# Performance work log

Hardware: AMD Instinct MI355X
Metric: run time of the kernel (lower is better)

The kernel has to match this reference:

```python
import jax, jax.numpy as jnp
import numpy as np

N, E, K, D = 100000, 3200000, 1024, 11


def setup_inputs() -> dict:
    key = jax.random.key(0)
    ks = jax.random.split(key, 11)
    return {
        "x": jax.random.normal(ks[0], (N, D), jnp.float32),
        "edge_index": jax.random.randint(ks[1], (2, E), 0, N, dtype=jnp.int32),
        "ready_idx": jnp.sort(jax.random.randint(ks[2], (K,), 0, N, dtype=jnp.int32)),
        "W1": jax.random.normal(ks[3], (D, 64), jnp.float32) * 0.2,
        "b1": jax.random.normal(ks[4], (64,), jnp.float32) * 0.02,
        "W2": jax.random.normal(ks[5], (75, 1), jnp.float32) * 0.2,
        "b2": jax.random.normal(ks[6], (1,), jnp.float32) * 0.02,
        "Wd": jax.random.normal(ks[7], (64, 1), jnp.float32) * 0.2,
        "bd": jax.random.normal(ks[8], (1,), jnp.float32) * 0.02,
        "Wv": jax.random.normal(ks[9], (64, 1), jnp.float32) * 0.2,
        "bv": jax.random.normal(ks[10], (1,), jnp.float32) * 0.02,
    }


def gcn_conv(x, W, b, src, dst):
    """PyG GCNConv with flow='target_to_source': gather from dst, aggregate at src.
    Symmetric normalization with self-loops (weight 1)."""
    n = x.shape[0]
    h = x @ W  # [N, F_out]
    loop = jnp.arange(n, dtype=src.dtype)
    s = jnp.concatenate([src, loop])  # aggregation index (row for target_to_source)
    d = jnp.concatenate([dst, loop])  # gather index
    deg = jax.ops.segment_sum(jnp.ones(s.shape, h.dtype), s, num_segments=n)
    dis = jnp.where(deg > 0, jax.lax.rsqrt(jnp.maximum(deg, 1e-12)), 0.0)
    norm = dis[s] * dis[d]  # [E+N]
    out = jax.ops.segment_sum(norm[:, None] * h[d], s, num_segments=n)
    return out + b


def reference(x, edge_index, ready_idx, W1, b1, W2, b2, Wd, bd, Wv, bv):
    src, dst = edge_index[0], edge_index[1]
    h = jax.nn.relu(gcn_conv(x, W1, b1, src, dst))           # [N, 64]
    x_input = jnp.concatenate([h, x], axis=1)                # [N, 75]
    probs_n = gcn_conv(x_input, W2, b2, src, dst)            # [N, 1]
    x_mean = jnp.mean(h, axis=0)                             # [64]
    v = x_mean @ Wv + bv                                     # [1]
    prob_nothing = x_mean @ Wd + bd                          # [1]
    logits = jnp.concatenate([probs_n[ready_idx, 0], prob_nothing])  # [K+1]
    probs = jax.nn.softmax(logits)
    return probs, v
```

## Files before the change

### kernel.cpp

```cpp
#include <hip/hip_runtime.h>
#include <hip/hip_fp16.h>
#include <math.h>

#define N_ 100000
#define E_ 3200000
#define K_ 1024
#define D_ 11
#define NBUCK_ 391
#define NPAD_ (NBUCK_ * 256)
#define CAPB_ 16384
#define CAP_ 32
#define CAPW_ 33
#define GB_ 512
#define BT_ 1024
#define CHUNK_ 6256
#define SA_ 4
#define XC_ 32
#define RSEG_ 4096
#define RSTRIDE_ 16

static inline size_t align512(size_t x) { return (x + 511) & ~(size_t)511; }

__device__ inline float2 h2f(unsigned int u) {
    __half2 h = *reinterpret_cast<__half2*>(&u);
    return __half22float2(h);
}

__global__ __launch_bounds__(BT_) void k_bin(const int* __restrict__ src,
                                             const int* __restrict__ dst,
                                             int* __restrict__ bcur,
                                             int* __restrict__ gbuf) {
    __shared__ int sbuf[NBUCK_ * CAPW_];
    __shared__ int scnt[NBUCK_];
    int t = threadIdx.x;
    for (int b = t; b < NBUCK_; b += BT_) scnt[b] = 0;
    __syncthreads();
    long e0 = (long)blockIdx.x * CHUNK_;
    for (int r = 0; r < CHUNK_; r += BT_ * 8) {
        int off = r + t * 8;
        long i0 = e0 + off;
        if (off < CHUNK_ && i0 + 7 < E_) {
            int4 s0 = *(const int4*)(src + i0);
            int4 s1 = *(const int4*)(src + i0 + 4);
            int4 d0 = *(const int4*)(dst + i0);
            int4 d1 = *(const int4*)(dst + i0 + 4);
            int ss[8] = {s0.x, s0.y, s0.z, s0.w, s1.x, s1.y, s1.z, s1.w};
            int dd[8] = {d0.x, d0.y, d0.z, d0.w, d1.x, d1.y, d1.z, d1.w};
#pragma unroll
            for (int q = 0; q < 8; q++) {
                int b = ss[q] >> 8;
                int pack = ((ss[q] & 255) << 17) | dd[q];
                int pos = atomicAdd(&scnt[b], 1);
                if (pos < CAP_) sbuf[b * CAPW_ + pos] = pack;
                else gbuf[b * CAPB_ + atomicAdd(&bcur[b], 1)] = pack;
            }
        }
    }
    __syncthreads();
    for (int b = t; b < NBUCK_; b += BT_) {
        int c = min(scnt[b], CAP_);
        while (c >= 16) {
            int off = atomicAdd(&bcur[b], 16);
            int g = b * CAPB_ + off;
            c -= 16;
            if ((off & 3) == 0) {
                int4* gp = (int4*)(gbuf + g);
#pragma unroll
                for (int q = 0; q < 4; q++)
                    gp[q] = make_int4(sbuf[b*CAPW_ + c + 4*q],
                                      sbuf[b*CAPW_ + c + 4*q + 1],
                                      sbuf[b*CAPW_ + c + 4*q + 2],
                                      sbuf[b*CAPW_ + c + 4*q + 3]);
            } else {
                for (int k = 0; k < 16; k++) gbuf[g + k] = sbuf[b*CAPW_ + c + k];
            }
        }
        if (c > 0) {
            int g = b * CAPB_ + atomicAdd(&bcur[b], c);
            for (int k = 0; k < c; k++) gbuf[g + k] = sbuf[b*CAPW_ + k];
        }
    }
}

__global__ __launch_bounds__(1024) void k_deg(const int* __restrict__ bcur,
                                              const int* __restrict__ gbuf,
                                              const float* __restrict__ x,
                                              const int* __restrict__ ready,
                                              float* __restrict__ dis,
                                              __half* __restrict__ xh,
                                              unsigned char* __restrict__ flag,
                                              float* __restrict__ pr_raw,
                                              float* __restrict__ xpart,
                                              int* __restrict__ rcntp) {
    __shared__ int hist[256];
    int t = threadIdx.x, b = blockIdx.x;
    if (t < 256) hist[t] = 0;
    int gi = b * 1024 + t;
    if (gi < XC_ * 64) xpart[gi] = 0.f;
    if (gi < 32 * RSTRIDE_) rcntp[gi] = 0;
    __syncthreads();
    int base = b * CAPB_;
    int cnt = min(bcur[b], CAPB_);
    int p = t * 4;
    for (; p + 3 < cnt; p += 4096) {
        int4 v = *(const int4*)(gbuf + base + p);
        atomicAdd(&hist[v.x >> 17], 1);
        atomicAdd(&hist[v.y >> 17], 1);
        atomicAdd(&hist[v.z >> 17], 1);
        atomicAdd(&hist[v.w >> 17], 1);
    }
    if (p < cnt) {
        for (int q = p; q < cnt; q++) atomicAdd(&hist[gbuf[base + q] >> 17], 1);
    }
    __syncthreads();
    if (t < 256) {
        int node = (b << 8) + t;
        if (node < N_) {
            float dv = rsqrtf((float)(hist[t] + 1));
            dis[node] = dv;
            pr_raw[node] = 0.f;
            __half hh[16];
#pragma unroll
            for (int j = 0; j < D_; j++)
                hh[j] = __float2half_rn(x[(size_t)node * D_ + j]);
            hh[11] = __float2half_rn(dv);
#pragma unroll
            for (int j = 12; j < 16; j++) hh[j] = __float2half_rn(0.f);
            uint4* dst = (uint4*)(xh + (size_t)node * 16);
            dst[0] = *(uint4*)(hh);
            dst[1] = *(uint4*)(hh + 8);
            int lo = 0, hi = K_ - 1, f = 0;
            while (lo <= hi) {
                int mid = (lo + hi) >> 1;
                int v = ready[mid];
                if (v == node) { f = 1; break; }
                if (v < node) lo = mid + 1; else hi = mid - 1;
            }
            flag[node] = (unsigned char)f;
        }
    }
}

__global__ __launch_bounds__(256) void k_agg(const int* __restrict__ bcur,
                                             const int* __restrict__ gbuf,
                                             const __half* __restrict__ xh,
                                             const unsigned char* __restrict__ flag,
                                             float* __restrict__ upart,
                                             int* __restrict__ rcntp,
                                             int2* __restrict__ redge) {
    __shared__ int sorted[4096];
    __shared__ int hist[256];
    __shared__ int incl[256];
    __shared__ int offa[256];
    int t = threadIdx.x, b = blockIdx.x, s = blockIdx.y;
    hist[t] = 0;
    __syncthreads();
    int base = b * CAPB_;
    int cnt = min(bcur[b], CAPB_);
    int seg = (cnt + SA_ - 1) / SA_;
    int lo = s * seg, hi = min(lo + seg, cnt);
    int segn = hi - lo;
    int kmax = (segn + 255) >> 8;
    int pk[16], rk[16];
    for (int k = 0; k < kmax; k++) {
        int idx = lo + (k << 8) + t;
        if (idx < hi) {
            pk[k] = gbuf[base + idx];
            rk[k] = atomicAdd(&hist[pk[k] >> 17], 1);
        } else pk[k] = -1;
    }
    __syncthreads();
    incl[t] = hist[t];
    __syncthreads();
    for (int off = 1; off < 256; off <<= 1) {
        int v = (t >= off) ? incl[t - off] : 0;
        __syncthreads();
        incl[t] += v;
        __syncthreads();
    }
    offa[t] = incl[t] - hist[t];
    __syncthreads();
    for (int k = 0; k < kmax; k++) {
        if (pk[k] >= 0) sorted[offa[pk[k] >> 17] + rk[k]] = pk[k];
    }
    __syncthreads();
    int my_start = offa[t], my_cnt = hist[t];
    int node = (b << 8) + t;
    const uint4* xr = (const uint4*)xh;
    float acc[D_];
#pragma unroll
    for (int j = 0; j < D_; j++) acc[j] = 0.f;
    int i = 0;
    for (; i + 3 < my_cnt; i += 4) {
        int pp[4];
#pragma unroll
        for (int q = 0; q < 4; q++) pp[q] = sorted[my_start + i + q];
        uint4 A[4], B[4];
#pragma unroll
        for (int q = 0; q < 4; q++) {
            size_t r = (size_t)(pp[q] & 131071) * 2;
            A[q] = xr[r]; B[q] = xr[r + 1];
        }
#pragma unroll
        for (int q = 0; q < 4; q++) {
            float2 f0 = h2f(A[q].x), f1 = h2f(A[q].y), f2 = h2f(A[q].z);
            float2 f3 = h2f(A[q].w), f4 = h2f(B[q].x), f5 = h2f(B[q].y);
            float w = f5.y;
            acc[0]  = fmaf(w, f0.x, acc[0]);
            acc[1]  = fmaf(w, f0.y, acc[1]);
            acc[2]  = fmaf(w, f1.x, acc[2]);
            acc[3]  = fmaf(w, f1.y, acc[3]);
            acc[4]  = fmaf(w, f2.x, acc[4]);
            acc[5]  = fmaf(w, f2.y, acc[5]);
            acc[6]  = fmaf(w, f3.x, acc[6]);
            acc[7]  = fmaf(w, f3.y, acc[7]);
            acc[8]  = fmaf(w, f4.x, acc[8]);
            acc[9]  = fmaf(w, f4.y, acc[9]);
            acc[10] = fmaf(w, f5.x, acc[10]);
        }
    }
    for (; i < my_cnt; i++) {
        int pack = sorted[my_start + i];
        size_t r = (size_t)(pack & 131071) * 2;
        uint4 A = xr[r], B = xr[r + 1];
        float2 f0 = h2f(A.x), f1 = h2f(A.y), f2 = h2f(A.z);
        float2 f3 = h2f(A.w), f4 = h2f(B.x), f5 = h2f(B.y);
        float w = f5.y;
        acc[0]  = fmaf(w, f0.x, acc[0]);
        acc[1]  = fmaf(w, f0.y, acc[1]);
        acc[2]  = fmaf(w, f1.x, acc[2]);
        acc[3]  = fmaf(w, f1.y, acc[3]);
        acc[4]  = fmaf(w, f2.x, acc[4]);
        acc[5]  = fmaf(w, f2.y, acc[5]);
        acc[6]  = fmaf(w, f3.x, acc[6]);
        acc[7]  = fmaf(w, f3.y, acc[7]);
        acc[8]  = fmaf(w, f4.x, acc[8]);
        acc[9]  = fmaf(w, f4.y, acc[9]);
        acc[10] = fmaf(w, f5.x, acc[10]);
    }
    float* dst = upart + ((size_t)s * NPAD_ + node) * 12;
    ((float4*)dst)[0] = make_float4(acc[0], acc[1], acc[2],  acc[3]);
    ((float4*)dst)[1] = make_float4(acc[4], acc[5], acc[6],  acc[7]);
    ((float4*)dst)[2] = make_float4(acc[8], acc[9], acc[10], 0.f);

    if (node < N_ && my_cnt > 0 && flag[node]) {
        int r = (b * SA_ + s) & 31;
        int slot = atomicAdd(&rcntp[r * RSTRIDE_], my_cnt);
        int lim = min(my_cnt, max(0, RSEG_ - slot));
        for (int i2 = 0; i2 < lim; i2++)
            redge[(r << 12) + slot + i2] =
                make_int2(node, sorted[my_start + i2] & 131071);
    }
}

__global__ __launch_bounds__(256) void k_node(
    const float* __restrict__ upart, const float* __restrict__ x,
    const float* __restrict__ dis,
    const float* __restrict__ W1, const float* __restrict__ b1,
    const float* __restrict__ W2,
    float* __restrict__ hd, float* __restrict__ xpart) {
    __shared__ float sW1[D_ * 64];
    __shared__ float sb1[64];
    __shared__ float sW2[75];
    __shared__ float smean[64];
    int t = threadIdx.x;
    for (int k = t; k < D_ * 64; k += 256) sW1[k] = W1[k];
    if (t < 64) { sb1[t] = b1[t]; smean[t] = 0.f; }
    if (t < 75) sW2[t] = W2[t];
    __syncthreads();

    int nl = t >> 2, q = t & 3;
    int node = blockIdx.x * 64 + nl;
    bool valid = node < N_;

    float4 mine = make_float4(0.f, 0.f, 0.f, 0.f);
    if (valid && q < 3) {
        const int TOT3 = NPAD_ * 3;
        int slot = node * 3 + q;
        const float4* up = (const float4*)upart;
        float4 a = up[slot];
#pragma unroll
        for (int s = 1; s < SA_; s++) {
            float4 v = up[(size_t)s * TOT3 + slot];
            a.x += v.x; a.y += v.y; a.z += v.z; a.w += v.w;
        }
        mine = a;
    }
    int lb = (t & 63) & ~3;
    float acc[D_];
    acc[0]  = __shfl(mine.x, lb);     acc[1]  = __shfl(mine.y, lb);
    acc[2]  = __shfl(mine.z, lb);     acc[3]  = __shfl(mine.w, lb);
    acc[4]  = __shfl(mine.x, lb + 1); acc[5]  = __shfl(mine.y, lb + 1);
    acc[6]  = __shfl(mine.z, lb + 1); acc[7]  = __shfl(mine.w, lb + 1);
    acc[8]  = __shfl(mine.x, lb + 2); acc[9]  = __shfl(mine.y, lb + 2);
    acc[10] = __shfl(mine.z, lb + 2);

    float hreg[16];
    float h2v = 0.f;
    float di = 0.f;
    if (valid) {
        di = dis[node];
        float xr_[D_], g[D_];
#pragma unroll
        for (int j = 0; j < D_; j++) xr_[j] = x[(size_t)node * D_ + j];
#pragma unroll
        for (int j = 0; j < D_; j++) g[j] = di * (acc[j] + di * xr_[j]);

        int fbase = q << 4;
#pragma unroll
        for (int j = 0; j < 16; j++) {
            int f = fbase + j;
            float a = sb1[f];
#pragma unroll
            for (int jj = 0; jj < D_; jj++) a = fmaf(g[jj], sW1[jj * 64 + f], a);
            float hf = fmaxf(a, 0.f);
            hreg[j] = hf;
            h2v = fmaf(hf, sW2[f], h2v);
        }
        if (q == 0) {
#pragma unroll
            for (int jj = 0; jj < D_; jj++) h2v = fmaf(xr_[jj], sW2[64 + jj], h2v);
        }
    } else {
#pragma unroll
        for (int j = 0; j < 16; j++) hreg[j] = 0.f;
    }
    h2v += __shfl_xor(h2v, 1);
    h2v += __shfl_xor(h2v, 2);
    if (valid && q == 0) hd[node] = di * h2v;

    int lane = t & 63;
#pragma unroll
    for (int j = 0; j < 16; j++) {
        float v = hreg[j];
        v += __shfl_xor(v, 4);
        v += __shfl_xor(v, 8);
        v += __shfl_xor(v, 16);
        v += __shfl_xor(v, 32);
        if (lane < 4) atomicAdd(&smean[(lane << 4) + j], v);
    }
    __syncthreads();
    if (t < 64) atomicAdd(&xpart[((blockIdx.x & (XC_ - 1)) << 6) + t], smean[t]);
}

__global__ void k_pr(const int* __restrict__ rcntp, const int2* __restrict__ redge,
                     const float* __restrict__ hd, float* __restrict__ pr_raw) {
    int idx = blockIdx.x * blockDim.x + threadIdx.x;
    int r = idx >> 12;
    int off = idx & (RSEG_ - 1);
    if (r < 32 && off < min(rcntp[r * RSTRIDE_], RSEG_)) {
        int2 e = redge[(r << 12) + off];
        atomicAdd(&pr_raw[e.x], hd[e.y]);
    }
}

__global__ __launch_bounds__(1024) void k_final(
    const int* __restrict__ ready, const float* __restrict__ dis,
    const float* __restrict__ hd, const float* __restrict__ pr_raw,
    const float* __restrict__ xpart,
    const float* __restrict__ b2,
    const float* __restrict__ Wd, const float* __restrict__ bd,
    const float* __restrict__ Wv, const float* __restrict__ bv,
    float* __restrict__ out) {
    __shared__ float xm[64];
    __shared__ float red[1024];
    __shared__ float s_max, s_sum, s_pn, s_v;
    int t = threadIdx.x;
    if (t < 64) {
        float s = 0.f;
#pragma unroll
        for (int c = 0; c < XC_; c++) s += xpart[(c << 6) + t];
        xm[t] = s * (1.0f / N_);
    }
    __syncthreads();
    if (t == 0) {
        float pn = bd[0], vv = bv[0];
        for (int f = 0; f < 64; f++) { pn += xm[f] * Wd[f]; vv += xm[f] * Wv[f]; }
        s_pn = pn; s_v = vv;
    }
    int r = ready[t];
    float dr = dis[r];
    float l = dr * (pr_raw[r] + hd[r]) + b2[0];
    __syncthreads();
    float pn = s_pn;
    red[t] = (t == 0) ? fmaxf(l, pn) : l;
    __syncthreads();
    for (int sft = 512; sft > 0; sft >>= 1) {
        if (t < sft) red[t] = fmaxf(red[t], red[t + sft]);
        __syncthreads();
    }
    if (t == 0) s_max = red[0];
    __syncthreads();
    float m = s_max;
    float el = expf(l - m);
    red[t] = el + ((t == 0) ? expf(pn - m) : 0.f);
    __syncthreads();
    for (int sft = 512; sft > 0; sft >>= 1) {
        if (t < sft) red[t] += red[t + sft];
        __syncthreads();
    }
    if (t == 0) s_sum = red[0];
    __syncthreads();
    float inv = 1.0f / s_sum;
    out[t] = el * inv;
    if (t == 0) {
        out[K_] = expf(pn - m) * inv;
        out[K_ + 1] = s_v;
    }
}

extern "C" void kernel_launch(void* const* d_in, const int* in_sizes, int n_in,
                              void* d_out, int out_size, void* d_ws, size_t ws_size,
                              hipStream_t stream) {
    const float* x    = (const float*)d_in[0];
    const int*   ei   = (const int*)d_in[1];
    const int*   src  = ei;
    const int*   dst  = ei + E_;
    const int*   ready= (const int*)d_in[2];
    const float* W1   = (const float*)d_in[3];
    const float* b1   = (const float*)d_in[4];
    const float* W2   = (const float*)d_in[5];
    const float* b2   = (const float*)d_in[6];
    const float* Wd   = (const float*)d_in[7];
    const float* bd   = (const float*)d_in[8];
    const float* Wv   = (const float*)d_in[9];
    const float* bv   = (const float*)d_in[10];
    float* out = (float*)d_out;

    char* ws = (char*)d_ws;
    size_t o = 0;
    int*   bcur   = (int*)(ws + o);          o += align512(NBUCK_ * sizeof(int));
    int*   rcntp  = (int*)(ws + o);          o += align512(32 * RSTRIDE_ * sizeof(int));
    int*   gbuf   = (int*)(ws + o);          o += align512((size_t)NBUCK_ * CAPB_ * sizeof(int));
    float* upart  = (float*)(ws + o);        o += align512((size_t)SA_ * NPAD_ * 12 * sizeof(float));
    __half* xh    = (__half*)(ws + o);       o += align512((size_t)N_ * 16 * sizeof(__half));
    int2*  redge  = (int2*)(ws + o);         o += align512((size_t)32 * RSEG_ * sizeof(int2));
    float* dis    = (float*)(ws + o);        o += align512(N_ * sizeof(float));
    float* hd     = (float*)(ws + o);        o += align512(N_ * sizeof(float));
    float* pr_raw = (float*)(ws + o);        o += align512(N_ * sizeof(float));
    unsigned char* flag = (unsigned char*)(ws + o); o += align512(N_);
    float* xpart  = (float*)(ws + o);        o += align512(XC_ * 64 * sizeof(float));

    const int B = 256;
    int g_node4 = (N_ + 63) / 64;
    int g_pr    = (32 * RSEG_) / B;
    dim3 gagg(NBUCK_, SA_);

    hipMemsetAsync(bcur, 0, NBUCK_ * sizeof(int), stream);
    k_bin  <<<GB_, BT_, 0, stream>>>(src, dst, bcur, gbuf);
    k_deg  <<<NBUCK_, 1024, 0, stream>>>(bcur, gbuf, x, ready, dis, xh, flag,
                                         pr_raw, xpart, rcntp);
    k_agg  <<<gagg, B, 0, stream>>>(bcur, gbuf, xh, flag, upart, rcntp, redge);
    k_node <<<g_node4, B, 0, stream>>>(upart, x, dis, W1, b1, W2, hd, xpart);
    k_pr   <<<g_pr, B, 0, stream>>>(rcntp, redge, hd, pr_raw);
    k_final<<<1, 1024, 0, stream>>>(ready, dis, hd, pr_raw, xpart,
                                    b2, Wd, bd, Wv, bv, out);
}
```

Baseline: 189.3 us.

## Fuse aggregation and node MLP into one 1024-thread per-bucket kernel

Merges k_agg and k_node into one kernel, k_agx. Each 1024-thread block handles a whole bucket of 256 nodes, with four threads per node splitting that node's edges and combining their partial sums through shuffles. This removes the upart partial-sum buffer (its write and re-read through global memory) and one kernel launch. It also recomputes the normalization from the shared histogram instead of loading dis. In exchange, the grid is only 391 large blocks that each need 64KB of shared memory for the sort buffer, which may limit occupancy. The sort switches to a two-pass scheme that reads gbuf twice.

```diff
diff --git a/kernel.cpp b/kernel.cpp
--- a/kernel.cpp
+++ b/kernel.cpp
@@ -14,7 +14,6 @@
 #define GB_ 512
 #define BT_ 1024
 #define CHUNK_ 6256
-#define SA_ 4
 #define XC_ 32
 #define RSEG_ 4096
 #define RSTRIDE_ 16
@@ -141,88 +140,62 @@
     }
 }
 
-__global__ __launch_bounds__(256) void k_agg(const int* __restrict__ bcur,
-                                             const int* __restrict__ gbuf,
-                                             const __half* __restrict__ xh,
-                                             const unsigned char* __restrict__ flag,
-                                             float* __restrict__ upart,
-                                             int* __restrict__ rcntp,
-                                             int2* __restrict__ redge) {
-    __shared__ int sorted[4096];
+__global__ __launch_bounds__(1024, 8) void k_agx(
+    const int* __restrict__ bcur, const int* __restrict__ gbuf,
+    const __half* __restrict__ xh, const float* __restrict__ x,
+    const unsigned char* __restrict__ flag,
+    const float* __restrict__ W1, const float* __restrict__ b1,
+    const float* __restrict__ W2,
+    float* __restrict__ hd, float* __restrict__ xpart,
+    int* __restrict__ rcntp, int2* __restrict__ redge) {
+    __shared__ int sorted[CAPB_];
     __shared__ int hist[256];
     __shared__ int incl[256];
     __shared__ int offa[256];
-    int t = threadIdx.x, b = blockIdx.x, s = blockIdx.y;
-    hist[t] = 0;
+    __shared__ int cur[256];
+    __shared__ float sW1[D_ * 64];
+    __shared__ float sb1[64];
+    __shared__ float sW2[75];
+    __shared__ float smean[64];
+    int t = threadIdx.x, b = blockIdx.x;
+    if (t < D_ * 64) sW1[t] = W1[t];
+    if (t >= 768 && t < 832) { sb1[t - 768] = b1[t - 768]; smean[t - 768] = 0.f; }
+    if (t >= 832 && t < 907) sW2[t - 832] = W2[t - 832];
+    if (t < 256) hist[t] = 0;
     __syncthreads();
     int base = b * CAPB_;
     int cnt = min(bcur[b], CAPB_);
-    int seg = (cnt + SA_ - 1) / SA_;
-    int lo = s * seg, hi = min(lo + seg, cnt);
-    int segn = hi - lo;
-    int kmax = (segn + 255) >> 8;
-    int pk[16], rk[16];
-    for (int k = 0; k < kmax; k++) {
-        int idx = lo + (k << 8) + t;
-        if (idx < hi) {
-            pk[k] = gbuf[base + idx];
-            rk[k] = atomicAdd(&hist[pk[k] >> 17], 1);
-        } else pk[k] = -1;
-    }
-    __syncthreads();
-    incl[t] = hist[t];
+    for (int idx = t; idx < cnt; idx += 1024)
+        atomicAdd(&hist[gbuf[base + idx] >> 17], 1);
+    __syncthreads();
+    if (t < 256) incl[t] = hist[t];
     __syncthreads();
     for (int off = 1; off < 256; off <<= 1) {
-        int v = (t >= off) ? incl[t - off] : 0;
+        int v = 0;
+        if (t < 256 && t >= off) v = incl[t - off];
         __syncthreads();
-        incl[t] += v;
+        if (t < 256) incl[t] += v;
         __syncthreads();
     }
-    offa[t] = incl[t] - hist[t];
-    __syncthreads();
-    for (int k = 0; k < kmax; k++) {
-        if (pk[k] >= 0) sorted[offa[pk[k] >> 17] + rk[k]] = pk[k];
-    }
-    __syncthreads();
-    int my_start = offa[t], my_cnt = hist[t];
-    int node = (b << 8) + t;
-    const uint4* xr = (const uint4*)xh;
+    if (t < 256) { int o = incl[t] - hist[t]; offa[t] = o; cur[t] = o; }
+    __syncthreads();
+    for (int idx = t; idx < cnt; idx += 1024) {
+        int pk = gbuf[base + idx];
+        sorted[atomicAdd(&cur[pk >> 17], 1)] = pk;
+    }
+    __syncthreads();
+    int nl = t >> 2, q = t & 3;
+    int node = (b << 8) + nl;
+    bool valid = node < N_;
+    int my_start = offa[nl], my_cnt = hist[nl];
+    const uint4* xr4 = (const uint4*)xh;
     float acc[D_];
 #pragma unroll
     for (int j = 0; j < D_; j++) acc[j] = 0.f;
-    int i = 0;
-    for (; i + 3 < my_cnt; i += 4) {
-        int pp[4];
-#pragma unroll
-        for (int q = 0; q < 4; q++) pp[q] = sorted[my_start + i + q];
-        uint4 A[4], B[4];
-#pragma unroll
-        for (int q = 0; q < 4; q++) {
-            size_t r = (size_t)(pp[q] & 131071) * 2;
-            A[q] = xr[r]; B[q] = xr[r + 1];
-        }
-#pragma unroll
-        for (int q = 0; q < 4; q++) {
-            float2 f0 = h2f(A[q].x), f1 = h2f(A[q].y), f2 = h2f(A[q].z);
-            float2 f3 = h2f(A[q].w), f4 = h2f(B[q].x), f5 = h2f(B[q].y);
-            float w = f5.y;
-            acc[0]  = fmaf(w, f0.x, acc[0]);
-            acc[1]  = fmaf(w, f0.y, acc[1]);
-            acc[2]  = fmaf(w, f1.x, acc[2]);
-            acc[3]  = fmaf(w, f1.y, acc[3]);
-            acc[4]  = fmaf(w, f2.x, acc[4]);
-            acc[5]  = fmaf(w, f2.y, acc[5]);
-            acc[6]  = fmaf(w, f3.x, acc[6]);
-            acc[7]  = fmaf(w, f3.y, acc[7]);
-            acc[8]  = fmaf(w, f4.x, acc[8]);
-            acc[9]  = fmaf(w, f4.y, acc[9]);
-            acc[10] = fmaf(w, f5.x, acc[10]);
-        }
-    }
-    for (; i < my_cnt; i++) {
+    for (int i = q; i < my_cnt; i += 4) {
         int pack = sorted[my_start + i];
         size_t r = (size_t)(pack & 131071) * 2;
-        uint4 A = xr[r], B = xr[r + 1];
+        uint4 A = xr4[r], B = xr4[r + 1];
         float2 f0 = h2f(A.x), f1 = h2f(A.y), f2 = h2f(A.z);
         float2 f3 = h2f(A.w), f4 = h2f(B.x), f5 = h2f(B.y);
         float w = f5.y;
@@ -238,74 +211,25 @@
         acc[9]  = fmaf(w, f4.y, acc[9]);
         acc[10] = fmaf(w, f5.x, acc[10]);
     }
-    float* dst = upart + ((size_t)s * NPAD_ + node) * 12;
-    ((float4*)dst)[0] = make_float4(acc[0], acc[1], acc[2],  acc[3]);
-    ((float4*)dst)[1] = make_float4(acc[4], acc[5], acc[6],  acc[7]);
-    ((float4*)dst)[2] = make_float4(acc[8], acc[9], acc[10], 0.f);
-
-    if (node < N_ && my_cnt > 0 && flag[node]) {
-        int r = (b * SA_ + s) & 31;
-        int slot = atomicAdd(&rcntp[r * RSTRIDE_], my_cnt);
-        int lim = min(my_cnt, max(0, RSEG_ - slot));
-        for (int i2 = 0; i2 < lim; i2++)
-            redge[(r << 12) + slot + i2] =
-                make_int2(node, sorted[my_start + i2] & 131071);
-    }
-}
-
-__global__ __launch_bounds__(256) void k_node(
-    const float* __restrict__ upart, const float* __restrict__ x,
-    const float* __restrict__ dis,
-    const float* __restrict__ W1, const float* __restrict__ b1,
-    const float* __restrict__ W2,
-    float* __restrict__ hd, float* __restrict__ xpart) {
-    __shared__ float sW1[D_ * 64];
-    __shared__ float sb1[64];
-    __shared__ float sW2[75];
-    __shared__ float smean[64];
-    int t = threadIdx.x;
-    for (int k = t; k < D_ * 64; k += 256) sW1[k] = W1[k];
-    if (t < 64) { sb1[t] = b1[t]; smean[t] = 0.f; }
-    if (t < 75) sW2[t] = W2[t];
-    __syncthreads();
-
-    int nl = t >> 2, q = t & 3;
-    int node = blockIdx.x * 64 + nl;
-    bool valid = node < N_;
-
-    float4 mine = make_float4(0.f, 0.f, 0.f, 0.f);
-    if (valid && q < 3) {
-        const int TOT3 = NPAD_ * 3;
-        int slot = node * 3 + q;
-        const float4* up = (const float4*)upart;
-        float4 a = up[slot];
-#pragma unroll
-        for (int s = 1; s < SA_; s++) {
-            float4 v = up[(size_t)s * TOT3 + slot];
-            a.x += v.x; a.y += v.y; a.z += v.z; a.w += v.w;
-        }
-        mine = a;
-    }
-    int lb = (t & 63) & ~3;
-    float acc[D_];
-    acc[0]  = __shfl(mine.x, lb);     acc[1]  = __shfl(mine.y, lb);
-    acc[2]  = __shfl(mine.z, lb);     acc[3]  = __shfl(mine.w, lb);
-    acc[4]  = __shfl(mine.x, lb + 1); acc[5]  = __shfl(mine.y, lb + 1);
-    acc[6]  = __shfl(mine.z, lb + 1); acc[7]  = __shfl(mine.w, lb + 1);
-    acc[8]  = __shfl(mine.x, lb + 2); acc[9]  = __shfl(mine.y, lb + 2);
-    acc[10] = __shfl(mine.z, lb + 2);
-
+#pragma unroll
+    for (int j = 0; j < D_; j++) {
+        acc[j] += __shfl_xor(acc[j], 1);
+        acc[j] += __shfl_xor(acc[j], 2);
+    }
     float hreg[16];
     float h2v = 0.f;
     float di = 0.f;
     if (valid) {
-        di = dis[node];
+        di = rsqrtf((float)(hist[nl] + 1));
         float xr_[D_], g[D_];
 #pragma unroll
         for (int j = 0; j < D_; j++) xr_[j] = x[(size_t)node * D_ + j];
+        if (q == 0) {
+#pragma unroll
+            for (int jj = 0; jj < D_; jj++) h2v = fmaf(xr_[jj], sW2[64 + jj], h2v);
+        }
 #pragma unroll
         for (int j = 0; j < D_; j++) g[j] = di * (acc[j] + di * xr_[j]);
-
         int fbase = q << 4;
 #pragma unroll
         for (int j = 0; j < 16; j++) {
@@ -316,10 +240,6 @@
             float hf = fmaxf(a, 0.f);
             hreg[j] = hf;
             h2v = fmaf(hf, sW2[f], h2v);
-        }
-        if (q == 0) {
-#pragma unroll
-            for (int jj = 0; jj < D_; jj++) h2v = fmaf(xr_[jj], sW2[64 + jj], h2v);
         }
     } else {
 #pragma unroll
@@ -340,7 +260,18 @@
         if (lane < 4) atomicAdd(&smean[(lane << 4) + j], v);
     }
     __syncthreads();
-    if (t < 64) atomicAdd(&xpart[((blockIdx.x & (XC_ - 1)) << 6) + t], smean[t]);
+    if (t < 64) atomicAdd(&xpart[((b & (XC_ - 1)) << 6) + t], smean[t]);
+
+    if (valid && my_cnt > 0 && flag[node]) {
+        int r = b & 31;
+        int slot = 0;
+        if (q == 0) slot = atomicAdd(&rcntp[r * RSTRIDE_], my_cnt);
+        slot = __shfl(slot, lane & ~3);
+        int lim = min(my_cnt, max(0, RSEG_ - slot));
+        for (int i2 = q; i2 < lim; i2 += 4)
+            redge[(r << 12) + slot + i2] =
+                make_int2(node, sorted[my_start + i2] & 131071);
+    }
 }
 
 __global__ void k_pr(const int* __restrict__ rcntp, const int2* __restrict__ redge,
@@ -432,7 +363,6 @@
     int*   bcur   = (int*)(ws + o);          o += align512(NBUCK_ * sizeof(int));
     int*   rcntp  = (int*)(ws + o);          o += align512(32 * RSTRIDE_ * sizeof(int));
     int*   gbuf   = (int*)(ws + o);          o += align512((size_t)NBUCK_ * CAPB_ * sizeof(int));
-    float* upart  = (float*)(ws + o);        o += align512((size_t)SA_ * NPAD_ * 12 * sizeof(float));
     __half* xh    = (__half*)(ws + o);       o += align512((size_t)N_ * 16 * sizeof(__half));
     int2*  redge  = (int2*)(ws + o);         o += align512((size_t)32 * RSEG_ * sizeof(int2));
     float* dis    = (float*)(ws + o);        o += align512(N_ * sizeof(float));
@@ -442,16 +372,14 @@
     float* xpart  = (float*)(ws + o);        o += align512(XC_ * 64 * sizeof(float));
 
     const int B = 256;
-    int g_node4 = (N_ + 63) / 64;
-    int g_pr    = (32 * RSEG_) / B;
-    dim3 gagg(NBUCK_, SA_);
+    int g_pr = (32 * RSEG_) / B;
 
     hipMemsetAsync(bcur, 0, NBUCK_ * sizeof(int), stream);
     k_bin  <<<GB_, BT_, 0, stream>>>(src, dst, bcur, gbuf);
     k_deg  <<<NBUCK_, 1024, 0, stream>>>(bcur, gbuf, x, ready, dis, xh, flag,
                                          pr_raw, xpart, rcntp);
-    k_agg  <<<gagg, B, 0, stream>>>(bcur, gbuf, xh, flag, upart, rcntp, redge);
-    k_node <<<g_node4, B, 0, stream>>>(upart, x, dis, W1, b1, W2, hd, xpart);
+    k_agx  <<<NBUCK_, 1024, 0, stream>>>(bcur, gbuf, xh, x, flag, W1, b1, W2,
+                                         hd, xpart, rcntp, redge);
     k_pr   <<<g_pr, B, 0, stream>>>(rcntp, redge, hd, pr_raw);
     k_final<<<1, 1024, 0, stream>>>(ready, dis, hd, pr_raw, xpart,
                                     b2, Wd, bd, Wv, bv, out);
```

Result: no change. 186.8 us (-1.3%).
